# Performance work log

Measured on AMD Instinct MI355X. Metric: run time of the kernel, lower is better.

Reference implementation:

```python
import jax, jax.numpy as jnp
import numpy as np

GRAPH = 50  # top-k neighbors


def setup_inputs() -> dict:
    key = jax.random.key(0)
    k1, k2, k3, k4, k5 = jax.random.split(key, 5)
    B, N, D, C = 2048, 50000, 256, 100
    return {
        "features": jax.random.normal(k1, (B, D), dtype=jnp.float32),
        "anchor_feature": jax.random.normal(k2, (N, D), dtype=jnp.float32),
        "labels": jax.random.randint(k3, (B,), 0, C),
        "t_labels": jax.random.randint(k4, (B,), 0, C),
        "anchor_label": jax.random.randint(k5, (N,), 0, C),
    }


def reference(features, anchor_feature, labels, t_labels, anchor_label):
    # mode == 'knn_sim', reduction=False; t_labels is unpacked but unused.
    # [B, N] dot-product similarity
    sim = jnp.matmul(features, anchor_feature.T)
    # top-k values and indices along anchor dim
    topk_vals, topk_idx = jax.lax.top_k(sim, GRAPH)  # [B, k]
    # label-match mask gathered at the top-k anchors (equivalent to
    # building the full [B, N] eq-mask then torch.gather along dim 1,
    # but gathers anchor labels first to avoid the dense mask)
    nn_labels = anchor_label[topk_idx]               # [B, k]
    mask_k = (labels[:, None] == nn_labels).astype(jnp.float32)
    mean_log_prob_pos = mask_k.sum(axis=1) / GRAPH   # [B]
    mean_sim = topk_vals.sum(axis=1) / GRAPH         # [B]
    # NaN scrub (x != x) -> 0, as in the torch code
    mean_log_prob_pos = jnp.where(jnp.isnan(mean_log_prob_pos), 0.0, mean_log_prob_pos)
    loss = -mean_log_prob_pos                        # [B] (reduction=False)
    return loss, mean_sim
```

## Files before the change

### kernel.cpp

```cpp
#include <hip/hip_runtime.h>
#include <math.h>

#define B_ROWS 2048
#define N_ANCH 50000
#define DIM    256
#define TOPK   50

#define BT 128
#define AT 256
#define KC 32
#define NCHUNK 8
#define NCH 16
#define CHUNK 3125
#define NTILES 13
#define NSAMP 4096
#define CAPG 2048

#define NRB (B_ROWS / BT)
#define TSF (NRB * 8 * 512)
#define TSA (NCH * NTILES * 8 * 1024)

typedef __attribute__((ext_vector_type(8))) short bf16x8;
typedef __attribute__((ext_vector_type(8))) unsigned short u16x8;
typedef __attribute__((ext_vector_type(4))) float f32x4;

#define OFF_B 0
#define OFF_A 16384
#define BUFB  24576
#define SMEM_BYTES (3 * BUFB)

__device__ __forceinline__ void gl_lds16(const void* g, void* l) {
    __builtin_amdgcn_global_load_lds(
        (const __attribute__((address_space(1))) unsigned int*)g,
        (__attribute__((address_space(3))) unsigned int*)l, 16, 0, 0);
}

template<int N>
__device__ __forceinline__ void wait_vmcnt() {
    asm volatile("s_waitcnt vmcnt(%0)" :: "n"(N) : "memory");
}
__device__ __forceinline__ void wait_lgkm0() {
    asm volatile("s_waitcnt lgkmcnt(0)" ::: "memory");
}
__device__ __forceinline__ void pipe_bar() {
    asm volatile("" ::: "memory");
    __builtin_amdgcn_s_barrier();
    asm volatile("" ::: "memory");
}

__device__ __forceinline__ unsigned short f2bf(float x) {
    unsigned u = __float_as_uint(x);
    u += 0x7FFFu + ((u >> 16) & 1u);
    return (unsigned short)(u >> 16);
}

__device__ __forceinline__ unsigned f2ord(float f) {
    unsigned u = __float_as_uint(f);
    return (u & 0x80000000u) ? ~u : (u | 0x80000000u);
}
__device__ __forceinline__ float ord2f(unsigned o) {
    return (o & 0x80000000u) ? __uint_as_float(o & 0x7FFFFFFFu) : __uint_as_float(~o);
}

__device__ __forceinline__ void cvt8(const float4 v0, const float4 v1,
                                     u16x8* H, u16x8* L) {
    float f[8] = {v0.x, v0.y, v0.z, v0.w, v1.x, v1.y, v1.z, v1.w};
    u16x8 h, l;
    #pragma unroll
    for (int j = 0; j < 8; ++j) {
        unsigned short hb = f2bf(f[j]);
        h[j] = hb;
        l[j] = f2bf(f[j] - __uint_as_float((unsigned)hb << 16));
    }
    *H = h; *L = l;
}

__global__ __launch_bounds__(256)
void split_pack_feat(const float* __restrict__ x,
                     unsigned short* __restrict__ hi,
                     unsigned short* __restrict__ lo)
{
    const int S  = blockIdx.x * 256 + threadIdx.x;
    const int s  = S & 511;
    const int c  = (S >> 9) & 7;
    const int rb = S >> 12;
    const int r  = s & 127;
    const int kq = s >> 7;
    const int row = (rb << 7) + r;
    const int k   = (c << 5) + (kq << 3);
    const float4* src = (const float4*)(x + (size_t)row * DIM + k);
    u16x8 H, L;
    cvt8(src[0], src[1], &H, &L);
    *(u16x8*)(hi + (size_t)S * 8) = H;
    *(u16x8*)(lo + (size_t)S * 8) = L;
}

__global__ __launch_bounds__(256)
void split_pack_anc(const float* __restrict__ x,
                    unsigned short* __restrict__ hi,
                    unsigned short* __restrict__ lo)
{
    const int S    = blockIdx.x * 256 + threadIdx.x;
    const int s    = S & 1023;
    const int c    = (S >> 10) & 7;
    const int tg   = S >> 13;
    const int cidx = tg / NTILES;
    const int tile = tg - cidx * NTILES;
    int a = cidx * CHUNK + (tile << 8) + (s & 255);
    if (a >= N_ANCH) a = N_ANCH - 1;
    const int k = (c << 5) + ((s >> 8) << 3);
    const float4* src = (const float4*)(x + (size_t)a * DIM + k);
    u16x8 H, L;
    cvt8(src[0], src[1], &H, &L);
    *(u16x8*)(hi + (size_t)S * 8) = H;
    *(u16x8*)(lo + (size_t)S * 8) = L;
}

#define STAGE_LOADS 3
__device__ __forceinline__ void stage_tile(unsigned char* sb,
                                           const unsigned short* __restrict__ Bsrc,
                                           const unsigned short* __restrict__ Asrc,
                                           int w, int lane)
{
    #pragma unroll
    for (int i = 0; i < 2; ++i) {
        const int t = (w << 1) + i;
        gl_lds16(Bsrc + ((size_t)t << 9) + (lane << 3), sb + OFF_B + (t << 10));
    }
    gl_lds16(Asrc + (((w << 6) + lane) << 3), sb + OFF_A + (w << 10));
}

__device__ __forceinline__ void compute_tile(const unsigned char* sb,
                                             int wm, int wn, int quad, int lx,
                                             f32x4 (&acc)[4][4])
{
    bf16x8 bf[4], af[4];
    #pragma unroll
    for (int tn = 0; tn < 4; ++tn) {
        const int a = (wn << 6) + (tn << 4) + lx;
        bf[tn] = *(const bf16x8*)(sb + OFF_B + (quad << 12) + (a << 4));
    }
    #pragma unroll
    for (int tm = 0; tm < 4; ++tm) {
        const int r = (wm << 6) + (tm << 4) + lx;
        af[tm] = *(const bf16x8*)(sb + OFF_A + (quad << 11) + (r << 4));
    }
    __builtin_amdgcn_s_setprio(1);
    #pragma unroll
    for (int tm = 0; tm < 4; ++tm)
        #pragma unroll
        for (int tn = 0; tn < 4; ++tn)
            acc[tm][tn] = __builtin_amdgcn_mfma_f32_16x16x32_bf16(af[tm], bf[tn], acc[tm][tn], 0, 0, 0);
    __builtin_amdgcn_s_setprio(0);
}


__global__ __launch_bounds__(512, 4)
void knn_sample_gemm(const unsigned short* __restrict__ pfhi,
                     const unsigned short* __restrict__ pflo,
                     const unsigned short* __restrict__ pahi,
                     const unsigned short* __restrict__ palo,
                     float* __restrict__ sims)
{
    __shared__ __align__(16) unsigned char sMem[SMEM_BYTES];

    const int tid  = threadIdx.x;
    const int w    = tid >> 6;
    const int lane = tid & 63;
    const int quad = lane >> 4;
    const int lx   = lane & 15;
    const int wm   = w >> 2;
    const int wn   = w & 3;

    const int id   = blockIdx.x;
    const int xcd  = id & 7;
    const int t    = id >> 3;
    const int rb   = t & 15;
    const int cidx = ((t >> 4) << 3) | xcd;
    const int rbase = rb * BT;
    const int tg    = cidx * NTILES;

    const unsigned short* Fp[3] = {pfhi, pflo, pfhi};
    const unsigned short* Bp[3] = {pahi, pahi, palo};

    auto bsrc = [&](int it) {
        return Bp[it >> 3] + (((size_t)(tg << 3)) + (it & 7)) * 8192;
    };
    auto asrc = [&](int it) {
        return Fp[it >> 3] + (((size_t)(rb << 3)) + (it & 7)) * 4096;
    };

    f32x4 acc[4][4];
    const f32x4 z = {0.f, 0.f, 0.f, 0.f};
    #pragma unroll
    for (int tm = 0; tm < 4; ++tm)
        #pragma unroll
        for (int tn = 0; tn < 4; ++tn) acc[tm][tn] = z;

    stage_tile(sMem + 0 * BUFB, bsrc(0), asrc(0), w, lane);
    stage_tile(sMem + 1 * BUFB, bsrc(1), asrc(1), w, lane);
    __syncthreads();

    for (int it = 0; it < 24; ++it) {
        if (it + 2 < 24)
            stage_tile(sMem + ((it + 2) % 3) * BUFB, bsrc(it + 2), asrc(it + 2), w, lane);
        compute_tile(sMem + (it % 3) * BUFB, wm, wn, quad, lx, acc);
        wait_lgkm0();
        if (it + 2 < 24)      wait_vmcnt<STAGE_LOADS>();
        else if (it + 1 < 24) wait_vmcnt<0>();
        pipe_bar();
    }

    #pragma unroll
    for (int tm = 0; tm < 4; ++tm)
        #pragma unroll
        for (int tn = 0; tn < 4; ++tn)
            #pragma unroll
            for (int reg = 0; reg < 4; ++reg) {
                int row = rbase + (wm << 6) + (tm << 4) + (quad << 2) + reg;
                int col = (wn << 6) + (tn << 4) + lx;
                sims[(size_t)row * NSAMP + cidx * AT + col] = acc[tm][tn][reg];
            }
}

__global__ __launch_bounds__(256)
void bisect_thresh(const float* __restrict__ sims,
                   uint2* __restrict__ cand, int* __restrict__ cnt,
                   float* __restrict__ Tarr)
{
    __shared__ float sv[NSAMP];
    __shared__ float s_rmin[4], s_rmax[4];
    __shared__ int   s_c, s_ns;

    const int row = blockIdx.x;
    const int tid = threadIdx.x;
    const int lane = tid & 63, w = tid >> 6;
    const unsigned long long below = (lane == 0) ? 0ull : (~0ull >> (64 - lane));

    const float4* S4 = (const float4*)(sims + (size_t)row * NSAMP);
    for (int i = tid; i < NSAMP / 4; i += 256) ((float4*)sv)[i] = S4[i];
    __syncthreads();

    float lmin = INFINITY, lmax = -INFINITY;
    for (int e0 = 0; e0 < NSAMP; e0 += 256) {
        float v = sv[e0 + tid];
        lmin = fminf(lmin, v); lmax = fmaxf(lmax, v);
    }
    #pragma unroll
    for (int off = 32; off; off >>= 1) {
        lmin = fminf(lmin, __shfl_down(lmin, off));
        lmax = fmaxf(lmax, __shfl_down(lmax, off));
    }
    if (lane == 0) { s_rmin[w] = lmin; s_rmax[w] = lmax; }
    __syncthreads();
    float lo = fminf(fminf(s_rmin[0], s_rmin[1]), fminf(s_rmin[2], s_rmin[3]));
    float mx = fmaxf(fmaxf(s_rmax[0], s_rmax[1]), fmaxf(s_rmax[2], s_rmax[3]));
    float hi = ord2f(f2ord(mx) + 1);
    int clo = NSAMP;
    for (int it = 0; it < 32 && clo > 64; ++it) {
        float mid = 0.5f * (lo + hi);
        if (tid == 0) s_c = 0;
        __syncthreads();
        int lc = 0;
        for (int e0 = 0; e0 < NSAMP; e0 += 256) lc += (sv[e0 + tid] >= mid);
        #pragma unroll
        for (int off = 32; off; off >>= 1) lc += __shfl_down(lc, off);
        if (lane == 0) atomicAdd(&s_c, lc);
        __syncthreads();
        int c = s_c;
        if (c >= TOPK) { lo = mid; clo = c; } else hi = mid;
        __syncthreads();
    }
    if (tid == 0) { Tarr[row] = lo; s_ns = 0; }
    __syncthreads();

    for (int e0 = 0; e0 < NSAMP; e0 += 256) {
        int e = e0 + tid;
        float v = sv[e];
        bool pred = (v >= lo);
        unsigned long long mk = __ballot(pred);
        int base = 0;
        if (lane == 0) base = atomicAdd(&s_ns, __popcll(mk));
        base = __shfl(base, 0);
        if (pred) {
            int ofs = base + __popcll(mk & below);
            int anchor = (e >> 8) * CHUNK + (e & 255);
            cand[(size_t)row * CAPG + ofs] = make_uint2(__float_as_uint(v), (unsigned)anchor);
        }
    }
    __syncthreads();
    if (tid == 0) cnt[row] = s_ns;
}

__global__ __launch_bounds__(512, 4)
void knn_mfma_append(const unsigned short* __restrict__ pfhi,
                     const unsigned short* __restrict__ pflo,
                     const unsigned short* __restrict__ pahi,
                     const unsigned short* __restrict__ palo,
                     const float* __restrict__ Tarr,
                     uint2* __restrict__ cand, int* __restrict__ cnt)
{
    __shared__ __align__(16) unsigned char sMem[SMEM_BYTES];
    __shared__ float s_T[BT];

    const int tid  = threadIdx.x;
    const int w    = tid >> 6;
    const int lane = tid & 63;
    const int quad = lane >> 4;
    const int lx   = lane & 15;
    const int wm   = w >> 2;
    const int wn   = w & 3;

    const int id   = blockIdx.x;
    const int xcd  = id & 7;
    const int t    = id >> 3;
    const int rb   = t & 15;
    const int gseq = t >> 4;
    const int g    = (gseq << 3) | xcd;
    const int cidx = g & 15;
    const int tile = 1 + (g >> 4);
    const int rbase = rb * BT;

    if (tid < BT) s_T[tid] = Tarr[rbase + tid];

    const unsigned short* Fp[3] = {pfhi, pflo, pfhi};
    const unsigned short* Bp[3] = {pahi, pahi, palo};

    auto bsrc = [&](int it) {
        return Bp[it >> 3] + (((size_t)((cidx * NTILES + tile) << 3)) + (it & 7)) * 8192;
    };
    auto asrc = [&](int it) {
        return Fp[it >> 3] + (((size_t)(rb << 3)) + (it & 7)) * 4096;
    };

    stage_tile(sMem + 0 * BUFB, bsrc(0), asrc(0), w, lane);
    stage_tile(sMem + 1 * BUFB, bsrc(1), asrc(1), w, lane);
    __syncthreads();

    float thr[4][4];
    #pragma unroll
    for (int tm = 0; tm < 4; ++tm)
        #pragma unroll
        for (int reg = 0; reg < 4; ++reg)
            thr[tm][reg] = s_T[(wm << 6) + (tm << 4) + (quad << 2) + reg];

    f32x4 acc[4][4];
    const f32x4 z = {0.f, 0.f, 0.f, 0.f};
    #pragma unroll
    for (int tm = 0; tm < 4; ++tm)
        #pragma unroll
        for (int tn = 0; tn < 4; ++tn) acc[tm][tn] = z;

    for (int it = 0; it < 24; ++it) {
        if (it + 2 < 24)
            stage_tile(sMem + ((it + 2) % 3) * BUFB, bsrc(it + 2), asrc(it + 2), w, lane);
        compute_tile(sMem + (it % 3) * BUFB, wm, wn, quad, lx, acc);
        wait_lgkm0();
        if (it + 2 < 24)      wait_vmcnt<STAGE_LOADS>();
        else if (it + 1 < 24) wait_vmcnt<0>();
        pipe_bar();
    }

    const int abase = cidx * CHUNK + tile * AT;
    const int valid = min(AT, CHUNK - tile * AT);

    #pragma unroll
    for (int tm = 0; tm < 4; ++tm)
        #pragma unroll
        for (int tn = 0; tn < 4; ++tn)
            #pragma unroll
            for (int reg = 0; reg < 4; ++reg) {
                const float v    = acc[tm][tn][reg];
                const int   aoff = (wn << 6) + (tn << 4) + lx;
                if (aoff < valid && v >= thr[tm][reg]) {
                    const int row = rbase + (wm << 6) + (tm << 4) + (quad << 2) + reg;
                    int slot = atomicAdd(&cnt[row], 1);
                    if (slot < CAPG)
                        cand[(size_t)row * CAPG + slot] =
                            make_uint2(__float_as_uint(v), (unsigned)(abase + aoff));
                }
            }
}

__global__ __launch_bounds__(256)
void knn_final(const uint2* __restrict__ cand, const int* __restrict__ cnt,
               const int* __restrict__ labels, const int* __restrict__ anchor_label,
               float* __restrict__ out)
{
    __shared__ float pv[CAPG];
    __shared__ int   pi[CAPG];
    __shared__ float fv[128];
    __shared__ int   fi[128];
    __shared__ float s_rmin[4], s_rmax[4];
    __shared__ int   s_c, s_m, s_cm;
    __shared__ float s_sum;

    const int row = blockIdx.x;
    const int tid = threadIdx.x;
    const int lane = tid & 63, w = tid >> 6;
    const unsigned long long below = (lane == 0) ? 0ull : (~0ull >> (64 - lane));

    if (tid == 0) { s_sum = 0.f; s_cm = 0; }

    int ns = cnt[row]; if (ns > CAPG) ns = CAPG;
    for (int e0 = 0; e0 < ns; e0 += 256) {
        int e = e0 + tid;
        if (e < ns) {
            uint2 c = cand[(size_t)row * CAPG + e];
            pv[e] = __uint_as_float(c.x); pi[e] = (int)c.y;
        }
    }
    __syncthreads();
    const int mylab = labels[row];

    float lmin = INFINITY, lmax = -INFINITY;
    for (int e0 = 0; e0 < ns; e0 += 256) {
        int e = e0 + tid;
        if (e < ns) { float v = pv[e]; lmin = fminf(lmin, v); lmax = fmaxf(lmax, v); }
    }
    #pragma unroll
    for (int off = 32; off; off >>= 1) {
        lmin = fminf(lmin, __shfl_down(lmin, off));
        lmax = fmaxf(lmax, __shfl_down(lmax, off));
    }
    if (lane == 0) { s_rmin[w] = lmin; s_rmax[w] = lmax; }
    __syncthreads();
    float lo = fminf(fminf(s_rmin[0], s_rmin[1]), fminf(s_rmin[2], s_rmin[3]));
    float mx = fmaxf(fmaxf(s_rmax[0], s_rmax[1]), fmaxf(s_rmax[2], s_rmax[3]));
    float hi = ord2f(f2ord(mx) + 1);
    int clo = ns;
    for (int it = 0; it < 32 && clo > 96; ++it) {
        float mid = 0.5f * (lo + hi);
        if (tid == 0) s_c = 0;
        __syncthreads();
        int lc = 0;
        for (int e0 = 0; e0 < ns; e0 += 256) {
            int e = e0 + tid;
            lc += (e < ns && pv[e] >= mid);
        }
        #pragma unroll
        for (int off = 32; off; off >>= 1) lc += __shfl_down(lc, off);
        if (lane == 0) atomicAdd(&s_c, lc);
        __syncthreads();
        int c = s_c;
        if (c >= TOPK) { lo = mid; clo = c; } else hi = mid;
        __syncthreads();
    }

    if (clo <= 96) {
        if (tid == 0) s_m = 0;
        __syncthreads();
        for (int e0 = 0; e0 < ns; e0 += 256) {
            int e = e0 + tid;
            bool pred = (e < ns) && (pv[e] >= lo);
            unsigned long long mk = __ballot(pred);
            int base = 0;
            if (lane == 0) base = atomicAdd(&s_m, __popcll(mk));
            base = __shfl(base, 0);
            if (pred) {
                int ofs = base + __popcll(mk & below);
                fv[ofs] = pv[e]; fi[ofs] = pi[e];
            }
        }
        __syncthreads();
        const int m = s_m;
        if (tid < m) {
            float v = fv[tid]; int id = fi[tid];
            int r = 0;
            for (int q = 0; q < m; ++q) {
                float vq = fv[q];
                r += (vq > v) || (vq == v && fi[q] < id);
            }
            if (r < TOPK) {
                atomicAdd(&s_sum, v);
                if (anchor_label[id] == mylab) atomicAdd(&s_cm, 1);
            }
        }
    } else {
        for (int e0 = 0; e0 < ns; e0 += 256) {
            int e = e0 + tid;
            if (e < ns) {
                float v = pv[e]; int id = pi[e];
                int r = 0;
                for (int q = 0; q < ns; ++q) {
                    float vq = pv[q];
                    r += (vq > v) || (vq == v && pi[q] < id);
                }
                if (r < TOPK) {
                    atomicAdd(&s_sum, v);
                    if (anchor_label[id] == mylab) atomicAdd(&s_cm, 1);
                }
            }
        }
    }
    __syncthreads();
    if (tid == 0) {
        float mlp = (float)s_cm / (float)TOPK;
        out[row]          = -mlp;
        out[B_ROWS + row] = s_sum / (float)TOPK;
    }
}

extern "C" void kernel_launch(void* const* d_in, const int* in_sizes, int n_in,
                              void* d_out, int out_size, void* d_ws, size_t ws_size,
                              hipStream_t stream)
{
    const float* feat         = (const float*)d_in[0];
    const float* anc          = (const float*)d_in[1];
    const int*   labels       = (const int*)d_in[2];
    const int*   anchor_label = (const int*)d_in[4];
    float* out = (float*)d_out;

    char* ws = (char*)d_ws;
    size_t off = 0;
    unsigned short* pfhi = (unsigned short*)(ws + off); off += (size_t)TSF * 16;
    unsigned short* pflo = (unsigned short*)(ws + off); off += (size_t)TSF * 16;
    unsigned short* pahi = (unsigned short*)(ws + off); off += (size_t)TSA * 16;
    unsigned short* palo = (unsigned short*)(ws + off); off += (size_t)TSA * 16;
    float* sims = (float*)(ws + off);        off += (size_t)B_ROWS * NSAMP * 4;
    uint2* cand = (uint2*)sims;
    int*   cnt  = (int*)(ws + off);          off += (size_t)B_ROWS * 4;
    float* Tarr = (float*)(ws + off);        off += (size_t)B_ROWS * 4;

    hipLaunchKernelGGL(split_pack_feat, dim3(TSF / 256), dim3(256), 0, stream,
                       feat, pfhi, pflo);
    hipLaunchKernelGGL(split_pack_anc, dim3(TSA / 256), dim3(256), 0, stream,
                       anc, pahi, palo);
    hipLaunchKernelGGL(knn_sample_gemm, dim3(256), dim3(512), 0, stream,
                       pfhi, pflo, pahi, palo, sims);
    hipLaunchKernelGGL(bisect_thresh, dim3(B_ROWS), dim3(256), 0, stream,
                       sims, cand, cnt, Tarr);
    hipLaunchKernelGGL(knn_mfma_append, dim3(3072), dim3(512), 0, stream,
                       pfhi, pflo, pahi, palo, Tarr, cand, cnt);
    hipLaunchKernelGGL(knn_final, dim3(B_ROWS), dim3(256), 0, stream,
                       cand, cnt, labels, anchor_label, out);
}
```

Before: 526.7 us.

## Split append GEMM into 128x128 half-tiles with 256-thread double-buffered blocks

```diff
diff --git a/kernel.cpp b/kernel.cpp
--- a/kernel.cpp
+++ b/kernel.cpp
@@ -13,6 +13,7 @@
 #define NCH 16
 #define CHUNK 3125
 #define NTILES 13
+#define NHT 23
 #define NSAMP 4096
 #define CAPG 2048
 
@@ -27,7 +28,11 @@
 #define OFF_B 0
 #define OFF_A 16384
 #define BUFB  24576
-#define SMEM_BYTES (3 * BUFB)
+#define SMEM_S (3 * BUFB)
+
+#define OFF_B2 0
+#define OFF_A2 8192
+#define BUF2   16384
 
 __device__ __forceinline__ void gl_lds16(const void* g, void* l) {
     __builtin_amdgcn_global_load_lds(
@@ -116,6 +121,7 @@
     *(u16x8*)(lo + (size_t)S * 8) = L;
 }
 
+
 #define STAGE_LOADS 3
 __device__ __forceinline__ void stage_tile(unsigned char* sb,
                                            const unsigned short* __restrict__ Bsrc,
@@ -153,7 +159,6 @@
             acc[tm][tn] = __builtin_amdgcn_mfma_f32_16x16x32_bf16(af[tm], bf[tn], acc[tm][tn], 0, 0, 0);
     __builtin_amdgcn_s_setprio(0);
 }
-
 
 __global__ __launch_bounds__(512, 4)
 void knn_sample_gemm(const unsigned short* __restrict__ pfhi,
@@ -162,7 +167,7 @@
                      const unsigned short* __restrict__ palo,
                      float* __restrict__ sims)
 {
-    __shared__ __align__(16) unsigned char sMem[SMEM_BYTES];
+    __shared__ __align__(16) unsigned char sMem[SMEM_S];
 
     const int tid  = threadIdx.x;
     const int w    = tid >> 6;
@@ -292,7 +297,47 @@
     if (tid == 0) cnt[row] = s_ns;
 }
 
-__global__ __launch_bounds__(512, 4)
+
+#define STAGE_LOADS2 4
+__device__ __forceinline__ void stage_tile2(unsigned char* sb,
+                                            const unsigned short* __restrict__ Bsrc,
+                                            const unsigned short* __restrict__ Asrc,
+                                            int w, int lane)
+{
+    #pragma unroll
+    for (int i = 0; i < 2; ++i) {
+        gl_lds16(Bsrc + (w << 11) + (i << 9) + (lane << 3),
+                 sb + OFF_B2 + (w << 11) + (i << 10));
+        gl_lds16(Asrc + (((w << 1) + i) << 9) + (lane << 3),
+                 sb + OFF_A2 + (((w << 1) + i) << 10));
+    }
+}
+
+__device__ __forceinline__ void compute_tile2(const unsigned char* sb,
+                                              int wm, int wn, int quad, int lx,
+                                              f32x4 (&acc)[4][4])
+{
+    bf16x8 bf[4], af[4];
+    #pragma unroll
+    for (int tn = 0; tn < 4; ++tn) {
+        const int a = (wn << 6) + (tn << 4) + lx;
+        bf[tn] = *(const bf16x8*)(sb + OFF_B2 + (quad << 11) + (a << 4));
+    }
+    #pragma unroll
+    for (int tm = 0; tm < 4; ++tm) {
+        const int r = (wm << 6) + (tm << 4) + lx;
+        af[tm] = *(const bf16x8*)(sb + OFF_A2 + (quad << 11) + (r << 4));
+    }
+    __builtin_amdgcn_s_setprio(1);
+    #pragma unroll
+    for (int tm = 0; tm < 4; ++tm)
+        #pragma unroll
+        for (int tn = 0; tn < 4; ++tn)
+            acc[tm][tn] = __builtin_amdgcn_mfma_f32_16x16x32_bf16(af[tm], bf[tn], acc[tm][tn], 0, 0, 0);
+    __builtin_amdgcn_s_setprio(0);
+}
+
+__global__ __launch_bounds__(256, 4)
 void knn_mfma_append(const unsigned short* __restrict__ pfhi,
                      const unsigned short* __restrict__ pflo,
                      const unsigned short* __restrict__ pahi,
@@ -300,7 +345,7 @@
                      const float* __restrict__ Tarr,
                      uint2* __restrict__ cand, int* __restrict__ cnt)
 {
-    __shared__ __align__(16) unsigned char sMem[SMEM_BYTES];
+    __shared__ __align__(16) unsigned char sMem[2 * BUF2];
     __shared__ float s_T[BT];
 
     const int tid  = threadIdx.x;
@@ -308,17 +353,19 @@
     const int lane = tid & 63;
     const int quad = lane >> 4;
     const int lx   = lane & 15;
-    const int wm   = w >> 2;
-    const int wn   = w & 3;
+    const int wm   = w >> 1;
+    const int wn   = w & 1;
 
     const int id   = blockIdx.x;
     const int xcd  = id & 7;
     const int t    = id >> 3;
     const int rb   = t & 15;
-    const int gseq = t >> 4;
-    const int g    = (gseq << 3) | xcd;
+    const int u    = t >> 4;
+    const int g    = (u << 3) | xcd;
     const int cidx = g & 15;
-    const int tile = 1 + (g >> 4);
+    const int ht   = g >> 4;
+    const int tile = 1 + (ht >> 1);
+    const int h    = ht & 1;
     const int rbase = rb * BT;
 
     if (tid < BT) s_T[tid] = Tarr[rbase + tid];
@@ -327,14 +374,14 @@
     const unsigned short* Bp[3] = {pahi, pahi, palo};
 
     auto bsrc = [&](int it) {
-        return Bp[it >> 3] + (((size_t)((cidx * NTILES + tile) << 3)) + (it & 7)) * 8192;
+        return Bp[it >> 3] + (((size_t)((cidx * NTILES + tile) << 3)) + (it & 7)) * 8192
+               + (h << 10);
     };
     auto asrc = [&](int it) {
         return Fp[it >> 3] + (((size_t)(rb << 3)) + (it & 7)) * 4096;
     };
 
-    stage_tile(sMem + 0 * BUFB, bsrc(0), asrc(0), w, lane);
-    stage_tile(sMem + 1 * BUFB, bsrc(1), asrc(1), w, lane);
+    stage_tile2(sMem, bsrc(0), asrc(0), w, lane);
     __syncthreads();
 
     float thr[4][4];
@@ -351,18 +398,23 @@
         #pragma unroll
         for (int tn = 0; tn < 4; ++tn) acc[tm][tn] = z;
 
+    int cur = 0;
     for (int it = 0; it < 24; ++it) {
-        if (it + 2 < 24)
-            stage_tile(sMem + ((it + 2) % 3) * BUFB, bsrc(it + 2), asrc(it + 2), w, lane);
-        compute_tile(sMem + (it % 3) * BUFB, wm, wn, quad, lx, acc);
+        if (it + 1 < 24) {
+            stage_tile2(sMem + (cur ^ 1) * BUF2, bsrc(it + 1), asrc(it + 1), w, lane);
+            wait_vmcnt<STAGE_LOADS2>();
+        } else {
+            wait_vmcnt<0>();
+        }
+        pipe_bar();
+        compute_tile2(sMem + cur * BUF2, wm, wn, quad, lx, acc);
         wait_lgkm0();
-        if (it + 2 < 24)      wait_vmcnt<STAGE_LOADS>();
-        else if (it + 1 < 24) wait_vmcnt<0>();
         pipe_bar();
-    }
-
-    const int abase = cidx * CHUNK + tile * AT;
-    const int valid = min(AT, CHUNK - tile * AT);
+        cur ^= 1;
+    }
+
+    const int abase = cidx * CHUNK + tile * AT + h * 128;
+    const int valid = min(128, CHUNK - (tile * AT + h * 128));
 
     #pragma unroll
     for (int tm = 0; tm < 4; ++tm)
@@ -530,7 +582,7 @@
                        pfhi, pflo, pahi, palo, sims);
     hipLaunchKernelGGL(bisect_thresh, dim3(B_ROWS), dim3(256), 0, stream,
                        sims, cand, cnt, Tarr);
-    hipLaunchKernelGGL(knn_mfma_append, dim3(3072), dim3(512), 0, stream,
+    hipLaunchKernelGGL(knn_mfma_append, dim3(16 * 16 * NHT * 8 / 8), dim3(256), 0, stream,
                        pfhi, pflo, pahi, palo, Tarr, cand, cnt);
     hipLaunchKernelGGL(knn_final, dim3(B_ROWS), dim3(256), 0, stream,
                        cand, cnt, labels, anchor_label, out);
```

Result: slower. 538.9 us (+2.3%).
